# Optimization experiments

Hardware: AMD Instinct MI355X
Metric: run time of the kernel (lower is better)

Reference implementation:

```python
import jax, jax.numpy as jnp
import numpy as np

WS = 7   # window_size
NH = 4   # num_head
EPS = 1e-5

def _rel_idx(ws):
    c = np.stack(np.meshgrid(np.arange(ws), np.arange(ws), indexing='ij')).reshape(2, -1)
    r = (c[:, :, None] - c[:, None, :]).transpose(1, 2, 0)
    r[..., 0] += ws - 1
    r[..., 1] += ws - 1
    r[..., 0] *= 2 * ws - 1
    return r.sum(-1)  # (ws^2, ws^2) int

def _shift_mask(ws, ps):
    # faithful to torch get_shift_mask: additive mask value is (1-eq)*1e-9 (as in source)
    wn = ps // ws
    ss = ws // 2
    rt = (np.arange(ps) + ss) // ws
    m = rt[:, None] * (ps // ws) + rt[None, :] + 1
    m = np.roll(m, (-ss, -ss), axis=(0, 1))
    m = m.reshape(wn, ws, wn, ws).transpose(0, 2, 1, 3).reshape(wn * wn, ws * ws)
    eq = (m[:, :, None] == m[:, None, :]).astype(np.float32)
    return (1.0 - eq) * 1e-9  # (num_windows, ws^2, ws^2)

def _ln(x, g, b):
    mu = x.mean(-1, keepdims=True)
    v = ((x - mu) ** 2).mean(-1, keepdims=True)
    return (x - mu) * jax.lax.rsqrt(v + EPS) * g + b

def _win_attn(x, wqkv, bqkv, wo, bo, table, mask):
    bs, S, D = x.shape
    hd = D // NH
    qkv = x @ wqkv.T + bqkv
    q, k, v = jnp.split(qkv, 3, axis=-1)
    def heads(t):
        return t.reshape(bs, S, NH, hd).transpose(0, 2, 1, 3).reshape(bs * NH, S, hd)
    q, k, v = heads(q), heads(k), heads(v)
    ridx = _rel_idx(WS).reshape(-1)
    bias = table[ridx].reshape(S, S, NH).transpose(2, 0, 1)  # (NH, S, S)
    scores = jnp.einsum('bqd,bkd->bqk', q, k) / np.sqrt(hd).astype(np.float32)
    scores = scores + jnp.tile(bias, (bs, 1, 1))
    if mask is not None:
        # source tiles mask head-major while q/k/v are batch-major; replicate faithfully
        scores = scores + jnp.tile(mask, (NH, 1, 1))
    p = jax.nn.softmax(scores, axis=-1)
    out = jnp.einsum('bqk,bkd->bqd', p, v)
    out = out.reshape(bs, NH, S, hd).transpose(0, 2, 1, 3).reshape(bs, S, D)
    return out @ wo.T + bo

def _forward(x, ln1_g, ln1_b, w_qkv1, b_qkv1, w_o1, b_o1, tbl1,
             ln2_g, ln2_b, w_mlp1, b_mlp1,
             ln3_g, ln3_b, w_qkv2, b_qkv2, w_o2, b_o2, tbl2,
             ln4_g, ln4_b, w_mlp2, b_mlp2):
    B, S, D = x.shape
    ps = int(np.sqrt(S))
    wn = ps // WS
    nw = wn * wn
    s2 = WS * WS
    ss = WS // 2
    # block 1: W-MSA (note: source's image2sequence is a plain reshape, no inverse transpose)
    y = _ln(x, ln1_g, ln1_b)
    y = y.reshape(B, wn, WS, wn, WS, D).transpose(0, 1, 3, 2, 4, 5).reshape(B * nw, s2, D)
    y = _win_attn(y, w_qkv1, b_qkv1, w_o1, b_o1, tbl1, None)
    y = y.reshape(B, S, D)
    x = x + y
    # mlp1
    y = _ln(x, ln2_g, ln2_b) @ w_mlp1.T + b_mlp1
    x = x + y
    # block 2: SW-MSA
    y = _ln(x, ln3_g, ln3_b)
    y = jnp.roll(y.reshape(B, ps, ps, D), (-ss, -ss), axis=(1, 2))
    y = y.reshape(B, wn, WS, wn, WS, D).transpose(0, 1, 3, 2, 4, 5).reshape(B * nw, s2, D)
    mask = jnp.tile(jnp.asarray(_shift_mask(WS, ps)), (B, 1, 1))
    y = _win_attn(y, w_qkv2, b_qkv2, w_o2, b_o2, tbl2, mask)
    y = y.reshape(B, wn, wn, WS, WS, D).transpose(0, 1, 3, 2, 4, 5).reshape(B, ps, ps, D)
    y = jnp.roll(y, (ss, ss), axis=(1, 2)).reshape(B, S, D)
    x = x + y
    # mlp2; source line `y + x + y` has no assignment, so the final residual is dropped
    y = _ln(x, ln4_g, ln4_b) @ w_mlp2.T + b_mlp2
    return y

def setup_inputs() -> dict:
    key = jax.random.key(0)
    ks = jax.random.split(key, 16)
    B, S, D = 64, 3136, 128
    T = (2 * WS - 1) ** 2  # 169
    f32 = jnp.float32
    inp = {
        'x': jax.random.normal(ks[0], (B, S, D), dtype=f32),
        'ln1_g': jnp.ones((D,), f32), 'ln1_b': jnp.zeros((D,), f32),
        'w_qkv1': jax.random.normal(ks[1], (3 * D, D), dtype=f32) * 0.02,
        'b_qkv1': jnp.zeros((3 * D,), f32),
        'w_o1': jax.random.normal(ks[2], (D, D), dtype=f32) * 0.02,
        'b_o1': jnp.zeros((D,), f32),
        'tbl1': jax.random.normal(ks[3], (T, NH), dtype=f32) * 0.02,
        'ln2_g': jnp.ones((D,), f32), 'ln2_b': jnp.zeros((D,), f32),
        'w_mlp1': jax.random.normal(ks[4], (D, D), dtype=f32) * 0.02,
        'b_mlp1': jnp.zeros((D,), f32),
        'ln3_g': jnp.ones((D,), f32), 'ln3_b': jnp.zeros((D,), f32),
        'w_qkv2': jax.random.normal(ks[5], (3 * D, D), dtype=f32) * 0.02,
        'b_qkv2': jnp.zeros((3 * D,), f32),
        'w_o2': jax.random.normal(ks[6], (D, D), dtype=f32) * 0.02,
        'b_o2': jnp.zeros((D,), f32),
        'tbl2': jax.random.normal(ks[7], (T, NH), dtype=f32) * 0.02,
        'ln4_g': jnp.ones((D,), f32), 'ln4_b': jnp.zeros((D,), f32),
        'w_mlp2': jax.random.normal(ks[8], (D, D), dtype=f32) * 0.02,
        'b_mlp2': jnp.zeros((D,), f32),
    }
    return inp

def reference(x, ln1_g, ln1_b, w_qkv1, b_qkv1, w_o1, b_o1, tbl1,
              ln2_g, ln2_b, w_mlp1, b_mlp1,
              ln3_g, ln3_b, w_qkv2, b_qkv2, w_o2, b_o2, tbl2,
              ln4_g, ln4_b, w_mlp2, b_mlp2):
    return _forward(x, ln1_g, ln1_b, w_qkv1, b_qkv1, w_o1, b_o1, tbl1,
                    ln2_g, ln2_b, w_mlp1, b_mlp1,
                    ln3_g, ln3_b, w_qkv2, b_qkv2, w_o2, b_o2, tbl2,
                    ln4_g, ln4_b, w_mlp2, b_mlp2)
```

## Files before the change

kernel.cpp:

```cpp
#include <hip/hip_runtime.h>
#include <hip/hip_bf16.h>
#include <stdint.h>

#define PS 56
#define S_ 3136
#define DIM 128
#define NTOK 200704

typedef __attribute__((ext_vector_type(8))) short short8;
typedef __attribute__((ext_vector_type(4))) float f32x4;

__device__ __forceinline__ uint32_t bfpack(float a, float b){
  uint32_t ua = __float_as_uint(a); ua = (ua + 0x7fffu + ((ua >> 16) & 1u)) >> 16;
  uint32_t ub = __float_as_uint(b); ub = (ub + 0x7fffu + ((ub >> 16) & 1u)) & 0xffff0000u;
  return ua | ub;
}
__device__ __forceinline__ uint16_t bf16of(float a){
  uint32_t ua = __float_as_uint(a);
  return (uint16_t)((ua + 0x7fffu + ((ua >> 16) & 1u)) >> 16);
}

__device__ __forceinline__ int win_map(int r, int shift) {
  int b = r / S_;
  int rem = r - b * S_;
  int w = rem / 49;
  int p = rem - w * 49;
  int i = p / 7, j = p - i * 7;
  int wr = w >> 3, wc = w & 7;
  int row = wr * 7 + i + shift; if (row >= PS) row -= PS;
  int col = wc * 7 + j + shift; if (col >= PS) col -= PS;
  return b * S_ + row * PS + col;
}

__global__ __launch_bounds__(256) void ln_k(const float* __restrict__ X,
                                            const float* __restrict__ g,
                                            const float* __restrict__ b,
                                            uint16_t* __restrict__ O) {
  int t = blockIdx.x * 4 + (threadIdx.x >> 6);
  int lane = threadIdx.x & 63;
  float2 v = *(const float2*)(X + (size_t)t * DIM + lane * 2);
  float s = v.x + v.y, sq = v.x * v.x + v.y * v.y;
  #pragma unroll
  for (int o = 32; o; o >>= 1) { s += __shfl_xor(s, o); sq += __shfl_xor(sq, o); }
  float mu = s * (1.0f / 128.0f);
  float rs = rsqrtf(sq * (1.0f / 128.0f) - mu * mu + 1e-5f);
  float2 gg = *(const float2*)(g + lane * 2);
  float2 bb = *(const float2*)(b + lane * 2);
  float a = (v.x - mu) * rs * gg.x + bb.x;
  float c = (v.y - mu) * rs * gg.y + bb.y;
  ((uint32_t*)O)[(size_t)t * 64 + lane] = bfpack(a, c);
}

__global__ __launch_bounds__(256) void wconv_k(
    const float* __restrict__ w0, const float* __restrict__ w1,
    const float* __restrict__ w2, const float* __restrict__ w3,
    const float* __restrict__ w4, const float* __restrict__ w5,
    uint16_t* __restrict__ out) {
  int i = blockIdx.x * 256 + threadIdx.x;
  float v;
  if      (i <  49152) v = w0[i];
  else if (i <  98304) v = w1[i -  49152];
  else if (i < 114688) v = w2[i -  98304];
  else if (i < 131072) v = w3[i - 114688];
  else if (i < 147456) v = w4[i - 131072];
  else                 v = w5[i - 147456];
  out[i] = bf16of(v);
}

template<bool RES, bool DOLN>
__global__ __launch_bounds__(256) void gemm_d(
    const uint16_t* __restrict__ A, const uint16_t* __restrict__ Wb,
    const float* __restrict__ bias, const float* __restrict__ Rsrc,
    float* __restrict__ Xout, const float* __restrict__ lng,
    const float* __restrict__ lnb, uint16_t* __restrict__ xbout)
{
  __shared__ float lnred[64][4][2];
  const int tid = threadIdx.x;
  const int lane = tid & 63;
  const int lanelow = lane & 15;
  const int quad = lane >> 4;
  const int w = tid >> 6;
  const int base = blockIdx.x * 64;

  short8 af[4][4];
  #pragma unroll
  for (int mt = 0; mt < 4; ++mt) {
    const uint16_t* arow = A + (size_t)(base + mt * 16 + lanelow) * DIM;
    #pragma unroll
    for (int k0 = 0; k0 < 4; ++k0)
      af[mt][k0] = *(const short8*)(arow + k0 * 32 + quad * 8);
  }
  f32x4 acc[4][2];
  #pragma unroll
  for (int mt = 0; mt < 4; ++mt)
    #pragma unroll
    for (int nt = 0; nt < 2; ++nt) acc[mt][nt] = (f32x4){0.f, 0.f, 0.f, 0.f};
  #pragma unroll
  for (int nt = 0; nt < 2; ++nt) {
    int wrow = w * 32 + nt * 16 + lanelow;
    const uint16_t* wr_ = Wb + (size_t)wrow * DIM;
    short8 bfr[4];
    #pragma unroll
    for (int k0 = 0; k0 < 4; ++k0)
      bfr[k0] = *(const short8*)(wr_ + k0 * 32 + quad * 8);
    #pragma unroll
    for (int k0 = 0; k0 < 4; ++k0)
      #pragma unroll
      for (int mt = 0; mt < 4; ++mt)
        acc[mt][nt] = __builtin_amdgcn_mfma_f32_16x16x32_bf16(af[mt][k0], bfr[k0], acc[mt][nt], 0, 0, 0);
  }
  const int n0 = w * 32 + lanelow, n1 = n0 + 16;
  const float b0 = bias[n0], b1 = bias[n1];
  float g0, g1, e0, e1;
  if constexpr (DOLN) { g0 = lng[n0]; g1 = lng[n1]; e0 = lnb[n0]; e1 = lnb[n1]; }
  #pragma unroll
  for (int mt = 0; mt < 4; ++mt)
    #pragma unroll
    for (int r = 0; r < 4; ++r) {
      int row = mt * 16 + quad * 4 + r;
      int gm = base + row;
      float v0 = acc[mt][0][r] + b0;
      float v1 = acc[mt][1][r] + b1;
      if constexpr (RES) {
        v0 += Rsrc[(size_t)gm * DIM + n0];
        v1 += Rsrc[(size_t)gm * DIM + n1];
      }
      acc[mt][0][r] = v0; acc[mt][1][r] = v1;
      if constexpr (DOLN) {
        float s = v0 + v1, sq = v0 * v0 + v1 * v1;
        s += __shfl_xor(s, 1); sq += __shfl_xor(sq, 1);
        s += __shfl_xor(s, 2); sq += __shfl_xor(sq, 2);
        s += __shfl_xor(s, 4); sq += __shfl_xor(sq, 4);
        s += __shfl_xor(s, 8); sq += __shfl_xor(sq, 8);
        if (lanelow == 0) { lnred[row][w][0] = s; lnred[row][w][1] = sq; }
      } else {
        Xout[(size_t)gm * DIM + n0] = v0;
        Xout[(size_t)gm * DIM + n1] = v1;
      }
    }
  if constexpr (DOLN) {
    __syncthreads();
    #pragma unroll
    for (int mt = 0; mt < 4; ++mt)
      #pragma unroll
      for (int r = 0; r < 4; ++r) {
        int row = mt * 16 + quad * 4 + r;
        int gm = base + row;
        float s  = lnred[row][0][0] + lnred[row][1][0] + lnred[row][2][0] + lnred[row][3][0];
        float sq = lnred[row][0][1] + lnred[row][1][1] + lnred[row][2][1] + lnred[row][3][1];
        float mu = s * (1.0f / 128.0f);
        float rs = rsqrtf(sq * (1.0f / 128.0f) - mu * mu + 1e-5f);
        float v0 = acc[mt][0][r], v1 = acc[mt][1][r];
        Xout[(size_t)gm * DIM + n0] = v0;
        Xout[(size_t)gm * DIM + n1] = v1;
        xbout[(size_t)gm * DIM + n0] = bf16of((v0 - mu) * rs * g0 + e0);
        xbout[(size_t)gm * DIM + n1] = bf16of((v1 - mu) * rs * g1 + e1);
      }
  }
}

__global__ __launch_bounds__(256) void bias_k(const float* __restrict__ tbl, float* __restrict__ biasT) {
  int idx = blockIdx.x * 256 + threadIdx.x;
  int h = idx >> 12;
  int k = (idx >> 6) & 63;
  int q = idx & 63;
  float v;
  if (k >= 49)      v = -1e30f;
  else if (q >= 49) v = 0.f;
  else {
    int yi = q / 7, xi = q - yi * 7;
    int yj = k / 7, xj = k - yj * 7;
    v = tbl[((yi - yj + 6) * 13 + (xi - xj + 6)) * 4 + h];
  }
  biasT[idx] = v;
}

constexpr int QKSTR = 264;
constexpr int VSTR  = 72;
constexpr int OS_STR = 140;

template<int IN_SHIFT, int OUT_SHIFT>
__global__ __launch_bounds__(256) void attn3(const uint16_t* __restrict__ xbin,
                                             const uint16_t* __restrict__ Wqkv,
                                             const float* __restrict__ bqkv,
                                             const float* __restrict__ biasT,
                                             const uint16_t* __restrict__ Wo,
                                             const float* __restrict__ bo,
                                             const float* __restrict__ Rsrc,
                                             float* __restrict__ Xout,
                                             const float* __restrict__ lng,
                                             const float* __restrict__ lnb,
                                             uint16_t* __restrict__ xbout)
{
  __shared__ __align__(16) uint16_t qk_s[64 * QKSTR];
  __shared__ __align__(16) uint16_t vT[128 * VSTR];
  __shared__ float lnred[64][4][2];
  const int tid = threadIdx.x;
  const int lane = tid & 63;
  const int h = tid >> 6;
  const int lanelow = lane & 15;
  const int quad = lane >> 4;
  const int base = blockIdx.x * 49;

  {
    short8 af[4][4];
    #pragma unroll
    for (int mt = 0; mt < 4; ++mt) {
      int tok = mt * 16 + lanelow; if (tok > 48) tok = 48;
      int src = win_map(base + tok, IN_SHIFT);
      const uint16_t* arow = xbin + (size_t)src * DIM;
      #pragma unroll
      for (int k0 = 0; k0 < 4; ++k0)
        af[mt][k0] = *(const short8*)(arow + k0 * 32 + quad * 8);
    }
    #pragma unroll
    for (int ntl = 0; ntl < 4; ++ntl) {
      int dbase = (ntl >> 1) * 128 + h * 32 + (ntl & 1) * 16;
      const uint16_t* wr_ = Wqkv + (size_t)(dbase + lanelow) * DIM;
      short8 bfr[4];
      #pragma unroll
      for (int k0 = 0; k0 < 4; ++k0)
        bfr[k0] = *(const short8*)(wr_ + k0 * 32 + quad * 8);
      f32x4 a4[4];
      #pragma unroll
      for (int mt = 0; mt < 4; ++mt) a4[mt] = (f32x4){0.f, 0.f, 0.f, 0.f};
      #pragma unroll
      for (int k0 = 0; k0 < 4; ++k0)
        #pragma unroll
        for (int mt = 0; mt < 4; ++mt)
          a4[mt] = __builtin_amdgcn_mfma_f32_16x16x32_bf16(bfr[k0], af[mt][k0], a4[mt], 0, 0, 0);
      float4 bq4 = *(const float4*)(bqkv + dbase + quad * 4);
      #pragma unroll
      for (int mt = 0; mt < 4; ++mt) {
        uint2 pk;
        pk.x = bfpack(a4[mt][0] + bq4.x, a4[mt][1] + bq4.y);
        pk.y = bfpack(a4[mt][2] + bq4.z, a4[mt][3] + bq4.w);
        *(uint2*)(qk_s + (mt * 16 + lanelow) * QKSTR + dbase + quad * 4) = pk;
      }
    }
    #pragma unroll
    for (int ntl = 0; ntl < 2; ++ntl) {
      int wrow = 256 + h * 32 + ntl * 16 + lanelow;
      const uint16_t* wr_ = Wqkv + (size_t)wrow * DIM;
      short8 bfr[4];
      #pragma unroll
      for (int k0 = 0; k0 < 4; ++k0)
        bfr[k0] = *(const short8*)(wr_ + k0 * 32 + quad * 8);
      f32x4 a4[4];
      #pragma unroll
      for (int mt = 0; mt < 4; ++mt) a4[mt] = (f32x4){0.f, 0.f, 0.f, 0.f};
      #pragma unroll
      for (int k0 = 0; k0 < 4; ++k0)
        #pragma unroll
        for (int mt = 0; mt < 4; ++mt)
          a4[mt] = __builtin_amdgcn_mfma_f32_16x16x32_bf16(af[mt][k0], bfr[k0], a4[mt], 0, 0, 0);
      float bq = bqkv[wrow];
      int vd = h * 32 + ntl * 16 + lanelow;
      #pragma unroll
      for (int mt = 0; mt < 4; ++mt) {
        uint2 pk;
        pk.x = bfpack(a4[mt][0] + bq, a4[mt][1] + bq);
        pk.y = bfpack(a4[mt][2] + bq, a4[mt][3] + bq);
        *(uint2*)(vT + (size_t)vd * VSTR + mt * 16 + quad * 4) = pk;
      }
    }
  }

  const int n0 = h * 32 + lanelow, n1 = n0 + 16;
  int   orow_a[4][4];
  float r0a[4][4], r1a[4][4];
  #pragma unroll
  for (int qt = 0; qt < 4; ++qt)
    #pragma unroll
    for (int r = 0; r < 4; ++r) {
      int q = qt * 16 + quad * 4 + r;
      bool ok = (q < 49);
      int wrow = base + (ok ? q : 0);
      int orow = (OUT_SHIFT < 0) ? wrow : win_map(wrow, OUT_SHIFT);
      orow_a[qt][r] = orow;
      r0a[qt][r] = ok ? Rsrc[(size_t)orow * DIM + n0] : 0.f;
      r1a[qt][r] = ok ? Rsrc[(size_t)orow * DIM + n1] : 0.f;
    }

  f32x4 sc[4][4];
  #pragma unroll
  for (int kt = 0; kt < 4; ++kt)
    #pragma unroll
    for (int qt = 0; qt < 4; ++qt) sc[kt][qt] = (f32x4){0.f, 0.f, 0.f, 0.f};
  {
    short8 kf[4], qf[4];
    const int kcol = 128 + h * 32 + quad * 8;
    const int qcol = h * 32 + quad * 8;
    #pragma unroll
    for (int t = 0; t < 4; ++t) {
      int tok = t * 16 + lanelow; if (tok > 48) tok = 48;
      kf[t] = *(const short8*)(qk_s + tok * QKSTR + kcol);
      qf[t] = *(const short8*)(qk_s + tok * QKSTR + qcol);
    }
    __syncthreads();
    #pragma unroll
    for (int kt = 0; kt < 4; ++kt)
      #pragma unroll
      for (int qt = 0; qt < 4; ++qt)
        sc[kt][qt] = __builtin_amdgcn_mfma_f32_16x16x32_bf16(kf[kt], qf[qt], sc[kt][qt], 0, 0, 0);
  }

  const float* bh = biasT + h * 4096;
  #pragma unroll
  for (int kt = 0; kt < 4; ++kt)
    #pragma unroll
    for (int r = 0; r < 4; ++r) {
      const float* br = bh + (kt * 16 + quad * 4 + r) * 64 + lanelow;
      #pragma unroll
      for (int qt = 0; qt < 4; ++qt)
        sc[kt][qt][r] = fmaf(sc[kt][qt][r], 0.17677669529663689f, br[qt * 16]);
    }
  #pragma unroll
  for (int qt = 0; qt < 4; ++qt) {
    float m = sc[0][qt][0];
    #pragma unroll
    for (int kt = 0; kt < 4; ++kt)
      #pragma unroll
      for (int r = 0; r < 4; ++r) m = fmaxf(m, sc[kt][qt][r]);
    m = fmaxf(m, __shfl_xor(m, 16));
    m = fmaxf(m, __shfl_xor(m, 32));
    float s = 0.f;
    #pragma unroll
    for (int kt = 0; kt < 4; ++kt)
      #pragma unroll
      for (int r = 0; r < 4; ++r) {
        float e = __expf(sc[kt][qt][r] - m);
        sc[kt][qt][r] = e;
        s += e;
      }
    s += __shfl_xor(s, 16);
    s += __shfl_xor(s, 32);
    float inv = 1.0f / s;
    #pragma unroll
    for (int kt = 0; kt < 4; ++kt)
      #pragma unroll
      for (int r = 0; r < 4; ++r) sc[kt][qt][r] *= inv;
  }

  uint16_t* pw = qk_s + h * 64;
  #pragma unroll
  for (int qt = 0; qt < 4; ++qt)
    #pragma unroll
    for (int kt = 0; kt < 4; ++kt) {
      uint2 pk;
      pk.x = bfpack(sc[kt][qt][0], sc[kt][qt][1]);
      pk.y = bfpack(sc[kt][qt][2], sc[kt][qt][3]);
      *(uint2*)(pw + (qt * 16 + lanelow) * QKSTR + kt * 16 + quad * 4) = pk;
    }

  f32x4 oc[4][2];
  #pragma unroll
  for (int qt = 0; qt < 4; ++qt)
    #pragma unroll
    for (int dt = 0; dt < 2; ++dt) oc[qt][dt] = (f32x4){0.f, 0.f, 0.f, 0.f};
  {
    short8 pf[4][2];
    #pragma unroll
    for (int qt = 0; qt < 4; ++qt)
      #pragma unroll
      for (int kp = 0; kp < 2; ++kp)
        pf[qt][kp] = *(const short8*)(pw + (qt * 16 + lanelow) * QKSTR + kp * 32 + quad * 8);
    short8 vf[2][2];
    #pragma unroll
    for (int dt = 0; dt < 2; ++dt)
      #pragma unroll
      for (int kp = 0; kp < 2; ++kp)
        vf[dt][kp] = *(const short8*)(vT + (size_t)(h * 32 + dt * 16 + lanelow) * VSTR + kp * 32 + quad * 8);
    #pragma unroll
    for (int qt = 0; qt < 4; ++qt)
      #pragma unroll
      for (int dt = 0; dt < 2; ++dt)
        #pragma unroll
        for (int kp = 0; kp < 2; ++kp)
          oc[qt][dt] = __builtin_amdgcn_mfma_f32_16x16x32_bf16(pf[qt][kp], vf[dt][kp], oc[qt][dt], 0, 0, 0);
  }

  __syncthreads();
  uint16_t* Os = qk_s;
  #pragma unroll
  for (int qt = 0; qt < 4; ++qt)
    #pragma unroll
    for (int r = 0; r < 4; ++r) {
      int t = qt * 16 + quad * 4 + r;
      #pragma unroll
      for (int dt = 0; dt < 2; ++dt)
        Os[t * OS_STR + h * 32 + dt * 16 + lanelow] = bf16of(oc[qt][dt][r]);
    }
  __syncthreads();

  f32x4 rc[4][2];
  #pragma unroll
  for (int qt = 0; qt < 4; ++qt)
    #pragma unroll
    for (int dt = 0; dt < 2; ++dt) rc[qt][dt] = (f32x4){0.f, 0.f, 0.f, 0.f};
  #pragma unroll
  for (int kp = 0; kp < 4; ++kp) {
    short8 af[4];
    #pragma unroll
    for (int qt = 0; qt < 4; ++qt)
      af[qt] = *(const short8*)&Os[(qt * 16 + lanelow) * OS_STR + kp * 32 + quad * 8];
    short8 bfr[2];
    #pragma unroll
    for (int dt = 0; dt < 2; ++dt)
      bfr[dt] = *(const short8*)(Wo + (size_t)(h * 32 + dt * 16 + lanelow) * DIM + kp * 32 + quad * 8);
    #pragma unroll
    for (int qt = 0; qt < 4; ++qt)
      #pragma unroll
      for (int dt = 0; dt < 2; ++dt)
        rc[qt][dt] = __builtin_amdgcn_mfma_f32_16x16x32_bf16(af[qt], bfr[dt], rc[qt][dt], 0, 0, 0);
  }

  const float b0 = bo[n0], b1 = bo[n1];
  const float g0 = lng[n0], g1 = lng[n1];
  const float e0 = lnb[n0], e1 = lnb[n1];
  #pragma unroll
  for (int qt = 0; qt < 4; ++qt)
    #pragma unroll
    for (int r = 0; r < 4; ++r) {
      int q = qt * 16 + quad * 4 + r;
      float v0 = rc[qt][0][r] + b0 + r0a[qt][r];
      float v1 = rc[qt][1][r] + b1 + r1a[qt][r];
      rc[qt][0][r] = v0; rc[qt][1][r] = v1;
      float s = v0 + v1, sq = v0 * v0 + v1 * v1;
      s += __shfl_xor(s, 1); sq += __shfl_xor(sq, 1);
      s += __shfl_xor(s, 2); sq += __shfl_xor(sq, 2);
      s += __shfl_xor(s, 4); sq += __shfl_xor(sq, 4);
      s += __shfl_xor(s, 8); sq += __shfl_xor(sq, 8);
      if (lanelow == 0) { lnred[q][h][0] = s; lnred[q][h][1] = sq; }
    }
  __syncthreads();
  #pragma unroll
  for (int qt = 0; qt < 4; ++qt)
    #pragma unroll
    for (int r = 0; r < 4; ++r) {
      int q = qt * 16 + quad * 4 + r;
      if (q < 49) {
        int orow = orow_a[qt][r];
        float s  = lnred[q][0][0] + lnred[q][1][0] + lnred[q][2][0] + lnred[q][3][0];
        float sq = lnred[q][0][1] + lnred[q][1][1] + lnred[q][2][1] + lnred[q][3][1];
        float mu = s * (1.0f / 128.0f);
        float rs = rsqrtf(sq * (1.0f / 128.0f) - mu * mu + 1e-5f);
        float v0 = rc[qt][0][r], v1 = rc[qt][1][r];
        Xout[(size_t)orow * DIM + n0] = v0;
        Xout[(size_t)orow * DIM + n1] = v1;
        xbout[(size_t)orow * DIM + n0] = bf16of((v0 - mu) * rs * g0 + e0);
        xbout[(size_t)orow * DIM + n1] = bf16of((v1 - mu) * rs * g1 + e1);
      }
    }
}

extern "C" void kernel_launch(void* const* d_in, const int* in_sizes, int n_in,
                              void* d_out, int out_size, void* d_ws, size_t ws_size,
                              hipStream_t stream) {
  const float* x0    = (const float*)d_in[0];
  const float* ln1g  = (const float*)d_in[1];
  const float* ln1b  = (const float*)d_in[2];
  const float* wqkv1 = (const float*)d_in[3];
  const float* bqkv1 = (const float*)d_in[4];
  const float* wo1   = (const float*)d_in[5];
  const float* bo1   = (const float*)d_in[6];
  const float* tbl1  = (const float*)d_in[7];
  const float* ln2g  = (const float*)d_in[8];
  const float* ln2b  = (const float*)d_in[9];
  const float* wm1   = (const float*)d_in[10];
  const float* bm1   = (const float*)d_in[11];
  const float* ln3g  = (const float*)d_in[12];
  const float* ln3b  = (const float*)d_in[13];
  const float* wqkv2 = (const float*)d_in[14];
  const float* bqkv2 = (const float*)d_in[15];
  const float* wo2   = (const float*)d_in[16];
  const float* bo2   = (const float*)d_in[17];
  const float* tbl2  = (const float*)d_in[18];
  const float* ln4g  = (const float*)d_in[19];
  const float* ln4b  = (const float*)d_in[20];
  const float* wm2   = (const float*)d_in[21];
  const float* bm2   = (const float*)d_in[22];

  char* ws = (char*)d_ws;
  size_t off = 0;
  uint16_t* xbA  = (uint16_t*)(ws + off); off += (size_t)NTOK * 128 * sizeof(uint16_t);
  uint16_t* xb2  = (uint16_t*)(ws + off); off += (size_t)NTOK * 128 * sizeof(uint16_t);
  float* biasT1  = (float*)(ws + off);    off += 16384 * sizeof(float);
  float* biasT2  = (float*)(ws + off);    off += 16384 * sizeof(float);
  uint16_t* wb   = (uint16_t*)(ws + off); off += 163840 * sizeof(uint16_t);
  if (ws_size < off) return;
  float* x1 = (float*)d_out;

  uint16_t* wqkv1b = wb;
  uint16_t* wqkv2b = wb + 49152;
  uint16_t* wo1b   = wb + 98304;
  uint16_t* wm1b   = wb + 114688;
  uint16_t* wo2b   = wb + 131072;
  uint16_t* wm2b   = wb + 147456;

  dim3 blk(256);
  dim3 lgrid(NTOK / 4);
  dim3 dgrid(NTOK / 64);
  dim3 agrid(4096);

  wconv_k<<<640, blk, 0, stream>>>(wqkv1, wqkv2, wo1, wm1, wo2, wm2, wb);
  bias_k<<<64, blk, 0, stream>>>(tbl1, biasT1);
  bias_k<<<64, blk, 0, stream>>>(tbl2, biasT2);

  ln_k<<<lgrid, blk, 0, stream>>>(x0, ln1g, ln1b, xbA);
  attn3<0, -1><<<agrid, blk, 0, stream>>>(xbA, wqkv1b, bqkv1, biasT1, wo1b, bo1,
                                          x0, x1, ln2g, ln2b, xb2);
  gemm_d<true, true><<<dgrid, blk, 0, stream>>>(xb2, wm1b, bm1, x1, x1, ln3g, ln3b, xbA);
  attn3<3, 3><<<agrid, blk, 0, stream>>>(xbA, wqkv2b, bqkv2, biasT2, wo2b, bo2,
                                         x1, x1, ln4g, ln4b, xb2);
  gemm_d<false, false><<<dgrid, blk, 0, stream>>>(xb2, wm2b, bm2, nullptr, (float*)d_out,
                                                  nullptr, nullptr, nullptr);
}
```

Before: 698.1 us.

## Fuse MLP GEMM and following LayerNorm into windowed attention kernel

New measurement: 662.3 us. 1.05x faster.

```diff
diff --git a/kernel.cpp b/kernel.cpp
--- a/kernel.cpp
+++ b/kernel.cpp
@@ -67,98 +67,6 @@
   out[i] = bf16of(v);
 }
 
-template<bool RES, bool DOLN>
-__global__ __launch_bounds__(256) void gemm_d(
-    const uint16_t* __restrict__ A, const uint16_t* __restrict__ Wb,
-    const float* __restrict__ bias, const float* __restrict__ Rsrc,
-    float* __restrict__ Xout, const float* __restrict__ lng,
-    const float* __restrict__ lnb, uint16_t* __restrict__ xbout)
-{
-  __shared__ float lnred[64][4][2];
-  const int tid = threadIdx.x;
-  const int lane = tid & 63;
-  const int lanelow = lane & 15;
-  const int quad = lane >> 4;
-  const int w = tid >> 6;
-  const int base = blockIdx.x * 64;
-
-  short8 af[4][4];
-  #pragma unroll
-  for (int mt = 0; mt < 4; ++mt) {
-    const uint16_t* arow = A + (size_t)(base + mt * 16 + lanelow) * DIM;
-    #pragma unroll
-    for (int k0 = 0; k0 < 4; ++k0)
-      af[mt][k0] = *(const short8*)(arow + k0 * 32 + quad * 8);
-  }
-  f32x4 acc[4][2];
-  #pragma unroll
-  for (int mt = 0; mt < 4; ++mt)
-    #pragma unroll
-    for (int nt = 0; nt < 2; ++nt) acc[mt][nt] = (f32x4){0.f, 0.f, 0.f, 0.f};
-  #pragma unroll
-  for (int nt = 0; nt < 2; ++nt) {
-    int wrow = w * 32 + nt * 16 + lanelow;
-    const uint16_t* wr_ = Wb + (size_t)wrow * DIM;
-    short8 bfr[4];
-    #pragma unroll
-    for (int k0 = 0; k0 < 4; ++k0)
-      bfr[k0] = *(const short8*)(wr_ + k0 * 32 + quad * 8);
-    #pragma unroll
-    for (int k0 = 0; k0 < 4; ++k0)
-      #pragma unroll
-      for (int mt = 0; mt < 4; ++mt)
-        acc[mt][nt] = __builtin_amdgcn_mfma_f32_16x16x32_bf16(af[mt][k0], bfr[k0], acc[mt][nt], 0, 0, 0);
-  }
-  const int n0 = w * 32 + lanelow, n1 = n0 + 16;
-  const float b0 = bias[n0], b1 = bias[n1];
-  float g0, g1, e0, e1;
-  if constexpr (DOLN) { g0 = lng[n0]; g1 = lng[n1]; e0 = lnb[n0]; e1 = lnb[n1]; }
-  #pragma unroll
-  for (int mt = 0; mt < 4; ++mt)
-    #pragma unroll
-    for (int r = 0; r < 4; ++r) {
-      int row = mt * 16 + quad * 4 + r;
-      int gm = base + row;
-      float v0 = acc[mt][0][r] + b0;
-      float v1 = acc[mt][1][r] + b1;
-      if constexpr (RES) {
-        v0 += Rsrc[(size_t)gm * DIM + n0];
-        v1 += Rsrc[(size_t)gm * DIM + n1];
-      }
-      acc[mt][0][r] = v0; acc[mt][1][r] = v1;
-      if constexpr (DOLN) {
-        float s = v0 + v1, sq = v0 * v0 + v1 * v1;
-        s += __shfl_xor(s, 1); sq += __shfl_xor(sq, 1);
-        s += __shfl_xor(s, 2); sq += __shfl_xor(sq, 2);
-        s += __shfl_xor(s, 4); sq += __shfl_xor(sq, 4);
-        s += __shfl_xor(s, 8); sq += __shfl_xor(sq, 8);
-        if (lanelow == 0) { lnred[row][w][0] = s; lnred[row][w][1] = sq; }
-      } else {
-        Xout[(size_t)gm * DIM + n0] = v0;
-        Xout[(size_t)gm * DIM + n1] = v1;
-      }
-    }
-  if constexpr (DOLN) {
-    __syncthreads();
-    #pragma unroll
-    for (int mt = 0; mt < 4; ++mt)
-      #pragma unroll
-      for (int r = 0; r < 4; ++r) {
-        int row = mt * 16 + quad * 4 + r;
-        int gm = base + row;
-        float s  = lnred[row][0][0] + lnred[row][1][0] + lnred[row][2][0] + lnred[row][3][0];
-        float sq = lnred[row][0][1] + lnred[row][1][1] + lnred[row][2][1] + lnred[row][3][1];
-        float mu = s * (1.0f / 128.0f);
-        float rs = rsqrtf(sq * (1.0f / 128.0f) - mu * mu + 1e-5f);
-        float v0 = acc[mt][0][r], v1 = acc[mt][1][r];
-        Xout[(size_t)gm * DIM + n0] = v0;
-        Xout[(size_t)gm * DIM + n1] = v1;
-        xbout[(size_t)gm * DIM + n0] = bf16of((v0 - mu) * rs * g0 + e0);
-        xbout[(size_t)gm * DIM + n1] = bf16of((v1 - mu) * rs * g1 + e1);
-      }
-  }
-}
-
 __global__ __launch_bounds__(256) void bias_k(const float* __restrict__ tbl, float* __restrict__ biasT) {
   int idx = blockIdx.x * 256 + threadIdx.x;
   int h = idx >> 12;
@@ -175,25 +83,27 @@
   biasT[idx] = v;
 }
 
-constexpr int QKSTR = 264;
-constexpr int VSTR  = 72;
-constexpr int OS_STR = 140;
-
-template<int IN_SHIFT, int OUT_SHIFT>
-__global__ __launch_bounds__(256) void attn3(const uint16_t* __restrict__ xbin,
+constexpr int QKV_STR = 392;
+constexpr int OS_STR  = 140;
+
+template<int IN_SHIFT, int OUT_SHIFT, bool MLP_LN>
+__global__ __launch_bounds__(256) void attn4(const uint16_t* __restrict__ xbin,
                                              const uint16_t* __restrict__ Wqkv,
                                              const float* __restrict__ bqkv,
                                              const float* __restrict__ biasT,
                                              const uint16_t* __restrict__ Wo,
                                              const float* __restrict__ bo,
                                              const float* __restrict__ Rsrc,
+                                             const uint16_t* __restrict__ Wm,
+                                             const float* __restrict__ bm,
+                                             const float* __restrict__ lnga,
+                                             const float* __restrict__ lnba,
+                                             const float* __restrict__ lngp,
+                                             const float* __restrict__ lnbp,
                                              float* __restrict__ Xout,
-                                             const float* __restrict__ lng,
-                                             const float* __restrict__ lnb,
                                              uint16_t* __restrict__ xbout)
 {
-  __shared__ __align__(16) uint16_t qk_s[64 * QKSTR];
-  __shared__ __align__(16) uint16_t vT[128 * VSTR];
+  __shared__ __align__(16) uint16_t qs[64 * QKV_STR];
   __shared__ float lnred[64][4][2];
   const int tid = threadIdx.x;
   const int lane = tid & 63;
@@ -214,33 +124,8 @@
         af[mt][k0] = *(const short8*)(arow + k0 * 32 + quad * 8);
     }
     #pragma unroll
-    for (int ntl = 0; ntl < 4; ++ntl) {
-      int dbase = (ntl >> 1) * 128 + h * 32 + (ntl & 1) * 16;
-      const uint16_t* wr_ = Wqkv + (size_t)(dbase + lanelow) * DIM;
-      short8 bfr[4];
-      #pragma unroll
-      for (int k0 = 0; k0 < 4; ++k0)
-        bfr[k0] = *(const short8*)(wr_ + k0 * 32 + quad * 8);
-      f32x4 a4[4];
-      #pragma unroll
-      for (int mt = 0; mt < 4; ++mt) a4[mt] = (f32x4){0.f, 0.f, 0.f, 0.f};
-      #pragma unroll
-      for (int k0 = 0; k0 < 4; ++k0)
-        #pragma unroll
-        for (int mt = 0; mt < 4; ++mt)
-          a4[mt] = __builtin_amdgcn_mfma_f32_16x16x32_bf16(bfr[k0], af[mt][k0], a4[mt], 0, 0, 0);
-      float4 bq4 = *(const float4*)(bqkv + dbase + quad * 4);
-      #pragma unroll
-      for (int mt = 0; mt < 4; ++mt) {
-        uint2 pk;
-        pk.x = bfpack(a4[mt][0] + bq4.x, a4[mt][1] + bq4.y);
-        pk.y = bfpack(a4[mt][2] + bq4.z, a4[mt][3] + bq4.w);
-        *(uint2*)(qk_s + (mt * 16 + lanelow) * QKSTR + dbase + quad * 4) = pk;
-      }
-    }
-    #pragma unroll
-    for (int ntl = 0; ntl < 2; ++ntl) {
-      int wrow = 256 + h * 32 + ntl * 16 + lanelow;
+    for (int ntl = 0; ntl < 6; ++ntl) {
+      int wrow = (ntl >> 1) * 128 + h * 32 + (ntl & 1) * 16 + lanelow;
       const uint16_t* wr_ = Wqkv + (size_t)wrow * DIM;
       short8 bfr[4];
       #pragma unroll
@@ -255,14 +140,11 @@
         for (int mt = 0; mt < 4; ++mt)
           a4[mt] = __builtin_amdgcn_mfma_f32_16x16x32_bf16(af[mt][k0], bfr[k0], a4[mt], 0, 0, 0);
       float bq = bqkv[wrow];
-      int vd = h * 32 + ntl * 16 + lanelow;
-      #pragma unroll
-      for (int mt = 0; mt < 4; ++mt) {
-        uint2 pk;
-        pk.x = bfpack(a4[mt][0] + bq, a4[mt][1] + bq);
-        pk.y = bfpack(a4[mt][2] + bq, a4[mt][3] + bq);
-        *(uint2*)(vT + (size_t)vd * VSTR + mt * 16 + quad * 4) = pk;
-      }
+      #pragma unroll
+      for (int mt = 0; mt < 4; ++mt)
+        #pragma unroll
+        for (int r = 0; r < 4; ++r)
+          qs[(mt * 16 + quad * 4 + r) * QKV_STR + wrow] = bf16of(a4[mt][r] + bq);
     }
   }
 
@@ -294,8 +176,8 @@
     #pragma unroll
     for (int t = 0; t < 4; ++t) {
       int tok = t * 16 + lanelow; if (tok > 48) tok = 48;
-      kf[t] = *(const short8*)(qk_s + tok * QKSTR + kcol);
-      qf[t] = *(const short8*)(qk_s + tok * QKSTR + qcol);
+      kf[t] = *(const short8*)(qs + tok * QKV_STR + kcol);
+      qf[t] = *(const short8*)(qs + tok * QKV_STR + qcol);
     }
     __syncthreads();
     #pragma unroll
@@ -342,7 +224,7 @@
       for (int r = 0; r < 4; ++r) sc[kt][qt][r] *= inv;
   }
 
-  uint16_t* pw = qk_s + h * 64;
+  uint16_t* pw = qs + h * 64;
   #pragma unroll
   for (int qt = 0; qt < 4; ++qt)
     #pragma unroll
@@ -350,7 +232,7 @@
       uint2 pk;
       pk.x = bfpack(sc[kt][qt][0], sc[kt][qt][1]);
       pk.y = bfpack(sc[kt][qt][2], sc[kt][qt][3]);
-      *(uint2*)(pw + (qt * 16 + lanelow) * QKSTR + kt * 16 + quad * 4) = pk;
+      *(uint2*)(pw + (qt * 16 + lanelow) * QKV_STR + kt * 16 + quad * 4) = pk;
     }
 
   f32x4 oc[4][2];
@@ -364,13 +246,20 @@
     for (int qt = 0; qt < 4; ++qt)
       #pragma unroll
       for (int kp = 0; kp < 2; ++kp)
-        pf[qt][kp] = *(const short8*)(pw + (qt * 16 + lanelow) * QKSTR + kp * 32 + quad * 8);
+        pf[qt][kp] = *(const short8*)(pw + (qt * 16 + lanelow) * QKV_STR + kp * 32 + quad * 8);
     short8 vf[2][2];
     #pragma unroll
     for (int dt = 0; dt < 2; ++dt)
       #pragma unroll
-      for (int kp = 0; kp < 2; ++kp)
-        vf[dt][kp] = *(const short8*)(vT + (size_t)(h * 32 + dt * 16 + lanelow) * VSTR + kp * 32 + quad * 8);
+      for (int kp = 0; kp < 2; ++kp) {
+        short8 b;
+        #pragma unroll
+        for (int j = 0; j < 8; ++j) {
+          int tok = kp * 32 + quad * 8 + j; if (tok > 48) tok = 48;
+          b[j] = (short)qs[tok * QKV_STR + 256 + h * 32 + dt * 16 + lanelow];
+        }
+        vf[dt][kp] = b;
+      }
     #pragma unroll
     for (int qt = 0; qt < 4; ++qt)
       #pragma unroll
@@ -381,7 +270,7 @@
   }
 
   __syncthreads();
-  uint16_t* Os = qk_s;
+  uint16_t* Os = qs;
   #pragma unroll
   for (int qt = 0; qt < 4; ++qt)
     #pragma unroll
@@ -416,8 +305,8 @@
   }
 
   const float b0 = bo[n0], b1 = bo[n1];
-  const float g0 = lng[n0], g1 = lng[n1];
-  const float e0 = lnb[n0], e1 = lnb[n1];
+  const float ga0 = lnga[n0], ga1 = lnga[n1];
+  const float ea0 = lnba[n0], ea1 = lnba[n1];
   #pragma unroll
   for (int qt = 0; qt < 4; ++qt)
     #pragma unroll
@@ -434,24 +323,94 @@
       if (lanelow == 0) { lnred[q][h][0] = s; lnred[q][h][1] = sq; }
     }
   __syncthreads();
+
+  uint16_t* Xl = qs;
   #pragma unroll
   for (int qt = 0; qt < 4; ++qt)
     #pragma unroll
     for (int r = 0; r < 4; ++r) {
       int q = qt * 16 + quad * 4 + r;
-      if (q < 49) {
-        int orow = orow_a[qt][r];
-        float s  = lnred[q][0][0] + lnred[q][1][0] + lnred[q][2][0] + lnred[q][3][0];
-        float sq = lnred[q][0][1] + lnred[q][1][1] + lnred[q][2][1] + lnred[q][3][1];
-        float mu = s * (1.0f / 128.0f);
-        float rs = rsqrtf(sq * (1.0f / 128.0f) - mu * mu + 1e-5f);
-        float v0 = rc[qt][0][r], v1 = rc[qt][1][r];
-        Xout[(size_t)orow * DIM + n0] = v0;
-        Xout[(size_t)orow * DIM + n1] = v1;
-        xbout[(size_t)orow * DIM + n0] = bf16of((v0 - mu) * rs * g0 + e0);
-        xbout[(size_t)orow * DIM + n1] = bf16of((v1 - mu) * rs * g1 + e1);
+      float s  = lnred[q][0][0] + lnred[q][1][0] + lnred[q][2][0] + lnred[q][3][0];
+      float sq = lnred[q][0][1] + lnred[q][1][1] + lnred[q][2][1] + lnred[q][3][1];
+      float mu = s * (1.0f / 128.0f);
+      float rs = rsqrtf(sq * (1.0f / 128.0f) - mu * mu + 1e-5f);
+      Xl[q * OS_STR + n0] = bf16of((rc[qt][0][r] - mu) * rs * ga0 + ea0);
+      Xl[q * OS_STR + n1] = bf16of((rc[qt][1][r] - mu) * rs * ga1 + ea1);
+    }
+  __syncthreads();
+
+  f32x4 mc[4][2];
+  #pragma unroll
+  for (int qt = 0; qt < 4; ++qt)
+    #pragma unroll
+    for (int dt = 0; dt < 2; ++dt) mc[qt][dt] = (f32x4){0.f, 0.f, 0.f, 0.f};
+  #pragma unroll
+  for (int kp = 0; kp < 4; ++kp) {
+    short8 af2[4];
+    #pragma unroll
+    for (int qt = 0; qt < 4; ++qt)
+      af2[qt] = *(const short8*)&Xl[(qt * 16 + lanelow) * OS_STR + kp * 32 + quad * 8];
+    short8 wfr[2];
+    wfr[0] = *(const short8*)(Wm + (size_t)n0 * DIM + kp * 32 + quad * 8);
+    wfr[1] = *(const short8*)(Wm + (size_t)n1 * DIM + kp * 32 + quad * 8);
+    #pragma unroll
+    for (int qt = 0; qt < 4; ++qt)
+      #pragma unroll
+      for (int dt = 0; dt < 2; ++dt)
+        mc[qt][dt] = __builtin_amdgcn_mfma_f32_16x16x32_bf16(af2[qt], wfr[dt], mc[qt][dt], 0, 0, 0);
+  }
+  const float bm0 = bm[n0], bm1 = bm[n1];
+
+  if constexpr (MLP_LN) {
+    const float gp0 = lngp[n0], gp1 = lngp[n1];
+    const float ep0 = lnbp[n0], ep1 = lnbp[n1];
+    #pragma unroll
+    for (int qt = 0; qt < 4; ++qt)
+      #pragma unroll
+      for (int r = 0; r < 4; ++r) {
+        int q = qt * 16 + quad * 4 + r;
+        float v0 = rc[qt][0][r] + mc[qt][0][r] + bm0;
+        float v1 = rc[qt][1][r] + mc[qt][1][r] + bm1;
+        rc[qt][0][r] = v0; rc[qt][1][r] = v1;
+        float s = v0 + v1, sq = v0 * v0 + v1 * v1;
+        s += __shfl_xor(s, 1); sq += __shfl_xor(sq, 1);
+        s += __shfl_xor(s, 2); sq += __shfl_xor(sq, 2);
+        s += __shfl_xor(s, 4); sq += __shfl_xor(sq, 4);
+        s += __shfl_xor(s, 8); sq += __shfl_xor(sq, 8);
+        if (lanelow == 0) { lnred[q][h][0] = s; lnred[q][h][1] = sq; }
       }
-    }
+    __syncthreads();
+    #pragma unroll
+    for (int qt = 0; qt < 4; ++qt)
+      #pragma unroll
+      for (int r = 0; r < 4; ++r) {
+        int q = qt * 16 + quad * 4 + r;
+        if (q < 49) {
+          int orow = orow_a[qt][r];
+          float s  = lnred[q][0][0] + lnred[q][1][0] + lnred[q][2][0] + lnred[q][3][0];
+          float sq = lnred[q][0][1] + lnred[q][1][1] + lnred[q][2][1] + lnred[q][3][1];
+          float mu = s * (1.0f / 128.0f);
+          float rs = rsqrtf(sq * (1.0f / 128.0f) - mu * mu + 1e-5f);
+          float v0 = rc[qt][0][r], v1 = rc[qt][1][r];
+          Xout[(size_t)orow * DIM + n0] = v0;
+          Xout[(size_t)orow * DIM + n1] = v1;
+          xbout[(size_t)orow * DIM + n0] = bf16of((v0 - mu) * rs * gp0 + ep0);
+          xbout[(size_t)orow * DIM + n1] = bf16of((v1 - mu) * rs * gp1 + ep1);
+        }
+      }
+  } else {
+    #pragma unroll
+    for (int qt = 0; qt < 4; ++qt)
+      #pragma unroll
+      for (int r = 0; r < 4; ++r) {
+        int q = qt * 16 + quad * 4 + r;
+        if (q < 49) {
+          int orow = orow_a[qt][r];
+          Xout[(size_t)orow * DIM + n0] = mc[qt][0][r] + bm0;
+          Xout[(size_t)orow * DIM + n1] = mc[qt][1][r] + bm1;
+        }
+      }
+  }
 }
 
 extern "C" void kernel_launch(void* const* d_in, const int* in_sizes, int n_in,
@@ -500,7 +459,6 @@
 
   dim3 blk(256);
   dim3 lgrid(NTOK / 4);
-  dim3 dgrid(NTOK / 64);
   dim3 agrid(4096);
 
   wconv_k<<<640, blk, 0, stream>>>(wqkv1, wqkv2, wo1, wm1, wo2, wm2, wb);
@@ -508,11 +466,10 @@
   bias_k<<<64, blk, 0, stream>>>(tbl2, biasT2);
 
   ln_k<<<lgrid, blk, 0, stream>>>(x0, ln1g, ln1b, xbA);
-  attn3<0, -1><<<agrid, blk, 0, stream>>>(xbA, wqkv1b, bqkv1, biasT1, wo1b, bo1,
-                                          x0, x1, ln2g, ln2b, xb2);
-  gemm_d<true, true><<<dgrid, blk, 0, stream>>>(xb2, wm1b, bm1, x1, x1, ln3g, ln3b, xbA);
-  attn3<3, 3><<<agrid, blk, 0, stream>>>(xbA, wqkv2b, bqkv2, biasT2, wo2b, bo2,
-                                         x1, x1, ln4g, ln4b, xb2);
-  gemm_d<false, false><<<dgrid, blk, 0, stream>>>(xb2, wm2b, bm2, nullptr, (float*)d_out,
-                                                  nullptr, nullptr, nullptr);
-}
+  attn4<0, -1, true><<<agrid, blk, 0, stream>>>(
+      xbA, wqkv1b, bqkv1, biasT1, wo1b, bo1, x0, wm1b, bm1,
+      ln2g, ln2b, ln3g, ln3b, x1, xb2);
+  attn4<3, 3, false><<<agrid, blk, 0, stream>>>(
+      xb2, wqkv2b, bqkv2, biasT2, wo2b, bo2, x1, wm2b, bm2,
+      ln4g, ln4b, ln4g, ln4b, x1, nullptr);
+}
```
